# Optimization experiments

Hardware: AMD Instinct MI355X
Metric: run time of the kernel (lower is better)

The kernel has to match this reference:

```python
import jax, jax.numpy as jnp
import numpy as np

N = 50000   # nodes
E = 800000  # edges (avg degree 16)
G = 64      # graphs in batch
H = 4       # attention heads
D = 128     # hidden dim per head (= hidden_dim)
V = 128     # embedding vocab (input_dim)
NEG_SLOPE = 0.2

def setup_inputs() -> dict:
    key = jax.random.key(0)
    ks = jax.random.split(key, 12)
    s = 0.05
    return {
        "feats": jax.random.randint(ks[0], (N,), 0, V),
        "src": jax.random.randint(ks[1], (E,), 0, N),
        "dst": jax.random.randint(ks[2], (E,), 0, N),
        "graph_ids": jnp.sort(jax.random.randint(ks[3], (N,), 0, G)),
        "emb": jax.random.normal(ks[4], (V, D)) * s,
        "W1": jax.random.normal(ks[5], (D, H * D)) * s,
        "b1": jax.random.normal(ks[6], (H * D,)) * s,
        "a1": jax.random.normal(ks[7], (H, D)) * s,
        "W2": jax.random.normal(ks[8], (D, H * D)) * s,
        "b2": jax.random.normal(ks[9], (H * D,)) * s,
        "a2": jax.random.normal(ks[10], (H, D)) * s,
        "Wreg": jax.random.normal(ks[11], (1, D)) * s,
    }

def gatv2_layer(x, W, b, a, src, dst):
    # shared-weight GATv2: h = Wx + b, split into heads -> [N,H,D]
    h = (x @ W + b).reshape(-1, H, D)
    hs = h[src]                      # [E,H,D] source feats per edge
    hd = h[dst]                      # [E,H,D] dest feats per edge
    e = jax.nn.leaky_relu(hs + hd, NEG_SLOPE)
    logits = jnp.einsum('ehd,hd->eh', e, a)          # [E,H]
    # edge softmax over incoming edges of each dst node
    m = jax.ops.segment_max(logits, dst, num_segments=N)
    m = jnp.where(jnp.isfinite(m), m, 0.0)           # empty segments -> 0 (unused)
    ex = jnp.exp(logits - m[dst])
    denom = jax.ops.segment_sum(ex, dst, num_segments=N)
    alpha = ex / denom[dst]                          # [E,H]
    rst = jax.ops.segment_sum(alpha[:, :, None] * hs, dst, num_segments=N)  # [N,H,D]
    return rst.mean(axis=1)          # .mean(dim=1) over heads -> [N,D]

def reference(feats, src, dst, graph_ids, emb, W1, b1, a1, W2, b2, a2, Wreg):
    x = emb[feats]                                   # embedding lookup [N,D]
    x = gatv2_layer(x, W1, b1, a1, src, dst)         # layer 1 (dropout=0)
    x = gatv2_layer(x, W2, b2, a2, src, dst)         # layer 2
    pooled = jax.ops.segment_sum(x, graph_ids, num_segments=G)  # SumPooling [G,D]
    return pooled @ Wreg.T                           # Linear bias=False -> [G,1]
```

## Files before the change

### kernel.cpp

```cpp
#include <hip/hip_runtime.h>
#include <hip/hip_bf16.h>

#define N_NODES 50000
#define N_EDGES 800000
#define G_GRAPHS 64
#define H_HEADS 4
#define D_DIM 128
#define HD 512
#define V_VOCAB 128
#define NEG_SLOPE 0.2f

typedef float f32x2v __attribute__((ext_vector_type(2)));
typedef float f32x4 __attribute__((ext_vector_type(4)));
typedef short s16x8 __attribute__((ext_vector_type(8)));
typedef _Float16 h16x2 __attribute__((ext_vector_type(2)));

static __device__ __forceinline__ float blo(unsigned int u) {
    union { float f; unsigned int i; } x; x.i = u << 16; return x.f;
}
static __device__ __forceinline__ float bhi(unsigned int u) {
    union { float f; unsigned int i; } x; x.i = u & 0xffff0000u; return x.f;
}
static __device__ __forceinline__ unsigned short f2b(float f) {
    union { float f; unsigned int i; } x; x.f = f;
    unsigned int r = x.i + 0x7fffu + ((x.i >> 16) & 1u);
    return (unsigned short)(r >> 16);
}
static __device__ __forceinline__ h16x2 u2h2(unsigned int u) {
    union { unsigned int u; h16x2 h; } c; c.u = u; return c.h;
}
static __device__ __forceinline__ unsigned int h22u(h16x2 h) {
    union { unsigned int u; h16x2 h; } c; c.h = h; return c.u;
}
static __device__ __forceinline__ h16x2 packf2(float lo, float hi) {
    union { __fp16 __attribute__((ext_vector_type(2))) p; h16x2 h; } c;
    c.p = __builtin_amdgcn_cvt_pkrtz(lo, hi);
    return c.h;
}

#if __has_builtin(__builtin_amdgcn_cvt_scalef32_pk_f16_fp8)
static __device__ __forceinline__ void fp8x4_to_h16(unsigned int u, h16x2& h0, h16x2& h1) {
    auto r0 = __builtin_amdgcn_cvt_scalef32_pk_f16_fp8((int)u, 1.0f, false);
    auto r1 = __builtin_amdgcn_cvt_scalef32_pk_f16_fp8((int)u, 1.0f, true);
    union { decltype(r0) p; h16x2 h; } c0, c1;
    c0.p = r0; c1.p = r1;
    h0 = c0.h; h1 = c1.h;
}
#else
static __device__ __forceinline__ void fp8x4_to_h16(unsigned int u, h16x2& h0, h16x2& h1) {
    f32x2v lo = __builtin_amdgcn_cvt_pk_f32_fp8(u, false);
    f32x2v hi = __builtin_amdgcn_cvt_pk_f32_fp8(u, true);
    h0 = packf2(lo.x, lo.y);
    h1 = packf2(hi.x, hi.y);
}
#endif

template<int CTRL>
static __device__ __forceinline__ float dpp_add(float v) {
    union { float f; int i; } a, b;
    a.f = v;
    b.i = __builtin_amdgcn_mov_dpp(a.i, CTRL, 0xF, 0xF, true);
    return v + b.f;
}
static __device__ __forceinline__ float row16_sum(float p) {
    p = dpp_add<0xB1>(p);
    p = dpp_add<0x4E>(p);
    p = dpp_add<0x141>(p);
    p = dpp_add<0x140>(p);
    return p;
}

__global__ void hist_kernel(const int* __restrict__ dst, int* __restrict__ counts,
                            float* __restrict__ pool) {
    if (blockIdx.x == 0 && threadIdx.x < G_GRAPHS) pool[threadIdx.x] = 0.f;
    int i = blockIdx.x * blockDim.x + threadIdx.x;
    if (i < N_EDGES) atomicAdd(&counts[dst[i]], 1);
}

__global__ void __launch_bounds__(256) scan1_kernel(const int* __restrict__ counts,
                                                    int* __restrict__ offsets,
                                                    int* __restrict__ bsum) {
    __shared__ int buf[256];
    int t = threadIdx.x, b = blockIdx.x;
    int i0 = (b * 256 + t) * 4;
    int v[4], c[4], s = 0;
    #pragma unroll
    for (int j = 0; j < 4; j++) {
        int idx = i0 + j;
        v[j] = (idx < N_NODES) ? counts[idx] : 0;
        s += v[j];
        c[j] = s;
    }
    buf[t] = s;
    __syncthreads();
    for (int off = 1; off < 256; off <<= 1) {
        int add = (t >= off) ? buf[t - off] : 0;
        __syncthreads();
        buf[t] += add;
        __syncthreads();
    }
    int ebase = (t > 0) ? buf[t - 1] : 0;
    #pragma unroll
    for (int j = 0; j < 4; j++) {
        int idx = i0 + j;
        if (idx < N_NODES) offsets[idx + 1] = ebase + c[j];
    }
    if (t == 0) bsum[b] = buf[255];
}

__global__ void __launch_bounds__(256) scan23_kernel(const int* __restrict__ counts,
                                                     int* __restrict__ offsets,
                                                     const int* __restrict__ bsum,
                                                     int* __restrict__ cursor) {
    __shared__ int sbase;
    int t = threadIdx.x, b = blockIdx.x;
    if (t < 64) {
        int v = (t < b) ? bsum[t] : 0;
        #pragma unroll
        for (int off = 1; off < 64; off <<= 1) v += __shfl_xor(v, off);
        if (t == 0) sbase = v;
    }
    __syncthreads();
    int base = sbase;
    int i0 = (b * 256 + t) * 4;
    #pragma unroll
    for (int j = 0; j < 4; j++) {
        int idx = i0 + j;
        if (idx < N_NODES) {
            int e = offsets[idx + 1] + base;
            offsets[idx + 1] = e;
            cursor[idx] = e - counts[idx];
        }
    }
    if (b == 0 && t == 0) offsets[0] = 0;
}

__global__ void scatter_kernel(const int* __restrict__ src, const int* __restrict__ dst,
                               int* __restrict__ cursor, int* __restrict__ csr_src) {
    int i = blockIdx.x * blockDim.x + threadIdx.x;
    if (i < N_EDGES) {
        int d = dst[i];
        int pos = atomicAdd(&cursor[d], 1);
        csr_src[pos] = src[i];
    }
}

__global__ void __launch_bounds__(256) prep_kernel(const float* __restrict__ emb,
                                                   const float* __restrict__ W1,
                                                   float* __restrict__ M1,
                                                   const float* __restrict__ W2,
                                                   unsigned short* __restrict__ Wb) {
    int b = blockIdx.x;
    if (b < 256) {
        int idx = b * 256 + threadIdx.x;
        int v = idx >> 9, c = idx & 511;
        float acc = 0.f;
        for (int k = 0; k < 128; k++)
            acc += emb[v * 128 + k] * W1[k * 512 + c];
        M1[idx] = acc;
    } else {
        int idx = (b - 256) * 256 + threadIdx.x;
        int j = idx & 7, c = (idx >> 3) & 511, qq = idx >> 12;
        Wb[idx] = f2b(W2[(qq * 8 + j) * 512 + c]);
    }
}

__global__ void gather_kernel(const int* __restrict__ feats, const float* __restrict__ M1,
                              const float* __restrict__ b1,
                              unsigned int* __restrict__ h) {
    int tid = blockIdx.x * blockDim.x + threadIdx.x;
    int i0 = tid * 8;
    int n = i0 >> 9, c = i0 & 511;
    if (n >= N_NODES) return;
    int f = feats[n];
    const float* mrow = &M1[f * 512 + c];
    float v[8];
    #pragma unroll
    for (int j = 0; j < 8; j++) v[j] = mrow[j] + b1[c + j];
    uint2 o;
    o.x = __builtin_amdgcn_cvt_pk_fp8_f32(v[0], v[1], 0, false);
    o.x = __builtin_amdgcn_cvt_pk_fp8_f32(v[2], v[3], o.x, true);
    o.y = __builtin_amdgcn_cvt_pk_fp8_f32(v[4], v[5], 0, false);
    o.y = __builtin_amdgcn_cvt_pk_fp8_f32(v[6], v[7], o.y, true);
    *reinterpret_cast<uint2*>(&h[i0 >> 2]) = o;
}

template<bool WRITE_DOTS>
__global__ void __launch_bounds__(256) gat_kernel(const unsigned int* __restrict__ h,
                                                  const int* __restrict__ offsets,
                                                  const int* __restrict__ csr_src,
                                                  const float* __restrict__ a,
                                                  const float* __restrict__ wreg,
                                                  unsigned short* __restrict__ x,
                                                  float* __restrict__ dots) {
    int wid = threadIdx.x >> 6;
    int lane = threadIdx.x & 63;
    int n = blockIdx.x * 4 + wid;
    if (n >= N_NODES) return;
    int row_s = offsets[n], row_e = offsets[n + 1];
    int cnt = row_e - row_s;

    h16x2 hd2[4], a06[4], a04[4], acc2[4];
    float pd;
    {
        uint2 hv = *reinterpret_cast<const uint2*>(&h[(size_t)n * 128 + lane * 2]);
        fp8x4_to_h16(hv.x, hd2[0], hd2[1]);
        fp8x4_to_h16(hv.y, hd2[2], hd2[3]);
        float4 av0 = *reinterpret_cast<const float4*>(&a[lane * 8]);
        float4 av1 = *reinterpret_cast<const float4*>(&a[lane * 8 + 4]);
        float aa[8] = {av0.x, av0.y, av0.z, av0.w, av1.x, av1.y, av1.z, av1.w};
        const float L2E = 1.4426950408889634f;
        #pragma unroll
        for (int k = 0; k < 4; k++) {
            a06[k][0] = (_Float16)(aa[2*k]   * (0.6f * L2E));
            a06[k][1] = (_Float16)(aa[2*k+1] * (0.6f * L2E));
            a04[k][0] = (_Float16)(aa[2*k]   * (0.4f * L2E));
            a04[k][1] = (_Float16)(aa[2*k+1] * (0.4f * L2E));
            acc2[k][0] = (_Float16)0.f; acc2[k][1] = (_Float16)0.f;
        }
        float s = 0.f;
        #pragma unroll
        for (int k = 0; k < 4; k++) s = __builtin_amdgcn_fdot2(hd2[k], a06[k], s, false);
        pd = row16_sum(s);
    }

    float den = 0.f;
    uint2 rA = make_uint2(0, 0), rB = make_uint2(0, 0);
    if (cnt > 0) {
        int s = csr_src[row_s];
        rA = *reinterpret_cast<const uint2*>(&h[(size_t)s * 128 + lane * 2]);
    }
    if (cnt > 1) {
        int s = csr_src[row_s + 1];
        rB = *reinterpret_cast<const uint2*>(&h[(size_t)s * 128 + lane * 2]);
    }

    const float C1 = 0.69314718f, C2 = 0.24022651f, C3 = 0.05550411f;

    auto process = [&](uint2 sv) {
        h16x2 hs[4];
        fp8x4_to_h16(sv.x, hs[0], hs[1]);
        fp8x4_to_h16(sv.y, hs[2], hs[3]);
        float p0 = 0.f, p1 = 0.f;
        #pragma unroll
        for (int k = 0; k < 2; k++) {
            h16x2 t2 = hs[k] + hd2[k];
            h16x2 at2 = u2h2(h22u(t2) & 0x7FFF7FFFu);
            p0 = __builtin_amdgcn_fdot2(hs[k], a06[k], p0, false);
            p0 = __builtin_amdgcn_fdot2(at2, a04[k], p0, false);
        }
        #pragma unroll
        for (int k = 2; k < 4; k++) {
            h16x2 t2 = hs[k] + hd2[k];
            h16x2 at2 = u2h2(h22u(t2) & 0x7FFF7FFFu);
            p1 = __builtin_amdgcn_fdot2(hs[k], a06[k], p1, false);
            p1 = __builtin_amdgcn_fdot2(at2, a04[k], p1, false);
        }
        float p = row16_sum(p0 + p1) + pd;
        float w = fmaf(p, fmaf(p, fmaf(p, C3, C2), C1), 1.f);
        den += w;
        h16x2 w2 = packf2(w, w);
        #pragma unroll
        for (int k = 0; k < 4; k++) acc2[k] = w2 * hs[k] + acc2[k];
    };

    for (int i = 0; i < cnt; i += 2) {
        {
            uint2 cur = rA;
            int nx = min(i + 2, cnt - 1);
            int s = csr_src[row_s + nx];
            rA = *reinterpret_cast<const uint2*>(&h[(size_t)s * 128 + lane * 2]);
            process(cur);
        }
        if (i + 1 < cnt) {
            uint2 cur = rB;
            int nx = min(i + 3, cnt - 1);
            int s = csr_src[row_s + nx];
            rB = *reinterpret_cast<const uint2*>(&h[(size_t)s * 128 + lane * 2]);
            process(cur);
        }
    }

    float inv = (den > 0.f) ? 0.25f / den : 0.f;
    float out8[8];
    #pragma unroll
    for (int j = 0; j < 8; j++) {
        float r = (float)acc2[j >> 1][j & 1] * inv;
        r += __shfl_xor(r, 16);
        r += __shfl_xor(r, 32);
        out8[j] = r;
    }
    if constexpr (WRITE_DOTS) {
        int d0 = (lane & 15) * 8;
        float4 wv0 = *reinterpret_cast<const float4*>(&wreg[d0]);
        float4 wv1 = *reinterpret_cast<const float4*>(&wreg[d0 + 4]);
        float pdot = out8[0] * wv0.x + out8[1] * wv0.y + out8[2] * wv0.z + out8[3] * wv0.w
                   + out8[4] * wv1.x + out8[5] * wv1.y + out8[6] * wv1.z + out8[7] * wv1.w;
        pdot = row16_sum(pdot);
        if (lane == 0) dots[n] = pdot;
    } else {
        if (lane < 16) {
            union { unsigned short u[8]; uint4 v; } o;
            #pragma unroll
            for (int j = 0; j < 8; j++) o.u[j] = f2b(out8[j]);
            *reinterpret_cast<uint4*>(&x[(size_t)n * 128 + lane * 8]) = o.v;
        }
    }
}

__global__ void __launch_bounds__(256) gemm_kernel(const unsigned short* __restrict__ x,
                                                   const unsigned short* __restrict__ Wb,
                                                   const float* __restrict__ bias,
                                                   unsigned char* __restrict__ hout) {
    int w = threadIdx.x >> 6, l = threadIdx.x & 63;
    int rb = blockIdx.x * 64 + w * 16;
    int cb = blockIdx.y * 64;
    int lr = l & 15, lq = l >> 4;
    f32x4 acc[4] = {};
    int arow = rb + lr;
    bool rok = arow < N_NODES;
    #pragma unroll
    for (int s = 0; s < 4; s++) {
        s16x8 afr = {};
        if (rok) afr = *reinterpret_cast<const s16x8*>(&x[(size_t)arow * 128 + s * 32 + lq * 8]);
        #pragma unroll
        for (int sub = 0; sub < 4; sub++) {
            s16x8 bfr = *reinterpret_cast<const s16x8*>(
                &Wb[(((size_t)(s * 4 + lq) * 512) + cb + sub * 16 + lr) << 3]);
            acc[sub] = __builtin_amdgcn_mfma_f32_16x16x32_bf16(bfr, afr, acc[sub], 0, 0, 0);
        }
    }
    if (!rok) return;
    #pragma unroll
    for (int sub = 0; sub < 4; sub++) {
        int col0 = cb + sub * 16 + lq * 4;
        float4 bb = *reinterpret_cast<const float4*>(&bias[col0]);
        unsigned int pk = __builtin_amdgcn_cvt_pk_fp8_f32(acc[sub][0] + bb.x,
                                                          acc[sub][1] + bb.y, 0, false);
        pk = __builtin_amdgcn_cvt_pk_fp8_f32(acc[sub][2] + bb.z,
                                             acc[sub][3] + bb.w, pk, true);
        *reinterpret_cast<unsigned int*>(&hout[(size_t)arow * 512 + col0]) = pk;
    }
}

__global__ void __launch_bounds__(256) pool64_kernel(const float* __restrict__ dots,
                                                     const int* __restrict__ gid,
                                                     float* __restrict__ pool) {
    int wave = (blockIdx.x * blockDim.x + threadIdx.x) >> 6;
    int lane = threadIdx.x & 63;
    int n0 = wave * 64;
    if (n0 >= N_NODES) return;
    int n = n0 + lane;
    int nc = min(n, N_NODES - 1);
    int g = gid[nc];
    float v = (n < N_NODES) ? dots[n] : 0.f;
    int g0 = __shfl(g, 0);
    bool uni = __all(g == g0);
    if (uni) {
        v += __shfl_xor(v, 1);
        v += __shfl_xor(v, 2);
        v += __shfl_xor(v, 4);
        v += __shfl_xor(v, 8);
        v += __shfl_xor(v, 16);
        v += __shfl_xor(v, 32);
        if (lane == 0) atomicAdd(&pool[g0], v);
    } else {
        if (n < N_NODES) atomicAdd(&pool[g], v);
    }
}

__global__ void final_kernel(const float* __restrict__ pool, float* __restrict__ out) {
    int t = threadIdx.x;
    if (t < G_GRAPHS) out[t] = pool[t];
}

extern "C" void kernel_launch(void* const* d_in, const int* in_sizes, int n_in,
                              void* d_out, int out_size, void* d_ws, size_t ws_size,
                              hipStream_t stream) {
    const int* feats = (const int*)d_in[0];
    const int* src   = (const int*)d_in[1];
    const int* dst   = (const int*)d_in[2];
    const int* gids  = (const int*)d_in[3];
    const float* emb  = (const float*)d_in[4];
    const float* W1   = (const float*)d_in[5];
    const float* b1   = (const float*)d_in[6];
    const float* a1   = (const float*)d_in[7];
    const float* W2   = (const float*)d_in[8];
    const float* b2   = (const float*)d_in[9];
    const float* a2   = (const float*)d_in[10];
    const float* wreg = (const float*)d_in[11];
    float* out = (float*)d_out;

    char* ws = (char*)d_ws;
    size_t off = 0;
    auto alloc = [&](size_t bytes) -> void* {
        void* p = ws + off;
        off = (off + bytes + 255) & ~(size_t)255;
        return p;
    };
    int*   counts  = (int*)alloc((size_t)N_NODES * 4);
    int*   offsets = (int*)alloc((size_t)(N_NODES + 1) * 4);
    int*   cursor  = (int*)alloc((size_t)N_NODES * 4);
    int*   csr_src = (int*)alloc((size_t)N_EDGES * 4);
    int*   bsum    = (int*)alloc(64 * 4);
    float* M1      = (float*)alloc((size_t)V_VOCAB * HD * 4);
    unsigned int*   h  = (unsigned int*)alloc((size_t)N_NODES * HD);
    unsigned short* x  = (unsigned short*)alloc((size_t)N_NODES * D_DIM * 2);
    unsigned short* Wb = (unsigned short*)alloc((size_t)D_DIM * HD * 2);
    float* dots    = (float*)alloc((size_t)N_NODES * 4);
    float* pool    = (float*)alloc((size_t)G_GRAPHS * 4);

    hipMemsetAsync(counts, 0, (size_t)N_NODES * 4, stream);

    hist_kernel<<<(N_EDGES + 255) / 256, 256, 0, stream>>>(dst, counts, pool);
    scan1_kernel<<<64, 256, 0, stream>>>(counts, offsets, bsum);
    scan23_kernel<<<64, 256, 0, stream>>>(counts, offsets, bsum, cursor);
    scatter_kernel<<<(N_EDGES + 255) / 256, 256, 0, stream>>>(src, dst, cursor, csr_src);

    prep_kernel<<<512, 256, 0, stream>>>(emb, W1, M1, W2, Wb);
    gather_kernel<<<(N_NODES * HD / 8) / 256, 256, 0, stream>>>(feats, M1, b1, h);

    gat_kernel<false><<<(N_NODES + 3) / 4, 256, 0, stream>>>(h, offsets, csr_src, a1,
                                                             wreg, x, dots);
    gemm_kernel<<<dim3((N_NODES + 63) / 64, 8), 256, 0, stream>>>(x, Wb, b2, (unsigned char*)h);
    gat_kernel<true><<<(N_NODES + 3) / 4, 256, 0, stream>>>(h, offsets, csr_src, a2,
                                                            wreg, x, dots);

    pool64_kernel<<<(N_NODES / 64 + 4) / 4, 256, 0, stream>>>(dots, gids, pool);
    final_kernel<<<1, 64, 0, stream>>>(pool, out);
}
```

Before: 362.9 us.

## Fold memset into prep kernel, fuse final copy into pool, scalarize GAT indices

Replaces the hipMemsetAsync of counts with extra blocks in prep_kernel, which is moved ahead of the histogram. It removes final_kernel by having the last block of pool64_kernel (found with an atomic done counter) write the output. In gat_kernel the node index, row offsets and neighbor indices become wave-uniform through readfirstlane, and 32-bit address math replaces size_t. Together these cut launch count and per-edge vector address work, at the cost of an atomic counter plus threadfence in the pooling kernel.

```diff
diff --git a/kernel.cpp b/kernel.cpp
--- a/kernel.cpp
+++ b/kernel.cpp
@@ -15,12 +15,6 @@
 typedef short s16x8 __attribute__((ext_vector_type(8)));
 typedef _Float16 h16x2 __attribute__((ext_vector_type(2)));
 
-static __device__ __forceinline__ float blo(unsigned int u) {
-    union { float f; unsigned int i; } x; x.i = u << 16; return x.f;
-}
-static __device__ __forceinline__ float bhi(unsigned int u) {
-    union { float f; unsigned int i; } x; x.i = u & 0xffff0000u; return x.f;
-}
 static __device__ __forceinline__ unsigned short f2b(float f) {
     union { float f; unsigned int i; } x; x.f = f;
     unsigned int r = x.i + 0x7fffu + ((x.i >> 16) & 1u);
@@ -145,23 +139,32 @@
     }
 }
 
+#define PREP_M1_BLOCKS   256
+#define PREP_WSZ_BLOCKS  256
+#define PREP_CNT_BLOCKS  196
 __global__ void __launch_bounds__(256) prep_kernel(const float* __restrict__ emb,
                                                    const float* __restrict__ W1,
                                                    float* __restrict__ M1,
                                                    const float* __restrict__ W2,
-                                                   unsigned short* __restrict__ Wb) {
+                                                   unsigned short* __restrict__ Wb,
+                                                   int* __restrict__ counts,
+                                                   int* __restrict__ done) {
     int b = blockIdx.x;
-    if (b < 256) {
+    if (b < PREP_M1_BLOCKS) {
         int idx = b * 256 + threadIdx.x;
         int v = idx >> 9, c = idx & 511;
         float acc = 0.f;
         for (int k = 0; k < 128; k++)
             acc += emb[v * 128 + k] * W1[k * 512 + c];
         M1[idx] = acc;
-    } else {
-        int idx = (b - 256) * 256 + threadIdx.x;
+    } else if (b < PREP_M1_BLOCKS + PREP_WSZ_BLOCKS) {
+        int idx = (b - PREP_M1_BLOCKS) * 256 + threadIdx.x;
         int j = idx & 7, c = (idx >> 3) & 511, qq = idx >> 12;
         Wb[idx] = f2b(W2[(qq * 8 + j) * 512 + c]);
+    } else {
+        int idx = (b - PREP_M1_BLOCKS - PREP_WSZ_BLOCKS) * 256 + threadIdx.x;
+        if (idx < N_NODES) counts[idx] = 0;
+        if (idx == 0) *done = 0;
     }
 }
 
@@ -197,13 +200,16 @@
     int lane = threadIdx.x & 63;
     int n = blockIdx.x * 4 + wid;
     if (n >= N_NODES) return;
-    int row_s = offsets[n], row_e = offsets[n + 1];
+    n = __builtin_amdgcn_readfirstlane(n);
+    int row_s = __builtin_amdgcn_readfirstlane(offsets[n]);
+    int row_e = __builtin_amdgcn_readfirstlane(offsets[n + 1]);
     int cnt = row_e - row_s;
+    int voff = lane * 2;
 
     h16x2 hd2[4], a06[4], a04[4], acc2[4];
     float pd;
     {
-        uint2 hv = *reinterpret_cast<const uint2*>(&h[(size_t)n * 128 + lane * 2]);
+        uint2 hv = *reinterpret_cast<const uint2*>(&h[(unsigned)n * 128u + voff]);
         fp8x4_to_h16(hv.x, hd2[0], hd2[1]);
         fp8x4_to_h16(hv.y, hd2[2], hd2[3]);
         float4 av0 = *reinterpret_cast<const float4*>(&a[lane * 8]);
@@ -224,16 +230,15 @@
         pd = row16_sum(s);
     }
 
+    auto ld = [&](int ii) {
+        int s = __builtin_amdgcn_readfirstlane(csr_src[row_s + ii]);
+        return *reinterpret_cast<const uint2*>(&h[(unsigned)s * 128u + voff]);
+    };
+
     float den = 0.f;
     uint2 rA = make_uint2(0, 0), rB = make_uint2(0, 0);
-    if (cnt > 0) {
-        int s = csr_src[row_s];
-        rA = *reinterpret_cast<const uint2*>(&h[(size_t)s * 128 + lane * 2]);
-    }
-    if (cnt > 1) {
-        int s = csr_src[row_s + 1];
-        rB = *reinterpret_cast<const uint2*>(&h[(size_t)s * 128 + lane * 2]);
-    }
+    if (cnt > 0) rA = ld(0);
+    if (cnt > 1) rB = ld(1);
 
     const float C1 = 0.69314718f, C2 = 0.24022651f, C3 = 0.05550411f;
 
@@ -267,16 +272,12 @@
     for (int i = 0; i < cnt; i += 2) {
         {
             uint2 cur = rA;
-            int nx = min(i + 2, cnt - 1);
-            int s = csr_src[row_s + nx];
-            rA = *reinterpret_cast<const uint2*>(&h[(size_t)s * 128 + lane * 2]);
+            rA = ld(min(i + 2, cnt - 1));
             process(cur);
         }
         if (i + 1 < cnt) {
             uint2 cur = rB;
-            int nx = min(i + 3, cnt - 1);
-            int s = csr_src[row_s + nx];
-            rB = *reinterpret_cast<const uint2*>(&h[(size_t)s * 128 + lane * 2]);
+            rB = ld(min(i + 3, cnt - 1));
             process(cur);
         }
     }
@@ -303,7 +304,7 @@
             union { unsigned short u[8]; uint4 v; } o;
             #pragma unroll
             for (int j = 0; j < 8; j++) o.u[j] = f2b(out8[j]);
-            *reinterpret_cast<uint4*>(&x[(size_t)n * 128 + lane * 8]) = o.v;
+            *reinterpret_cast<uint4*>(&x[(unsigned)n * 128u + lane * 8]) = o.v;
         }
     }
 }
@@ -345,33 +346,40 @@
 
 __global__ void __launch_bounds__(256) pool64_kernel(const float* __restrict__ dots,
                                                      const int* __restrict__ gid,
-                                                     float* __restrict__ pool) {
+                                                     float* __restrict__ pool,
+                                                     int* __restrict__ done,
+                                                     float* __restrict__ out) {
     int wave = (blockIdx.x * blockDim.x + threadIdx.x) >> 6;
     int lane = threadIdx.x & 63;
     int n0 = wave * 64;
-    if (n0 >= N_NODES) return;
-    int n = n0 + lane;
-    int nc = min(n, N_NODES - 1);
-    int g = gid[nc];
-    float v = (n < N_NODES) ? dots[n] : 0.f;
-    int g0 = __shfl(g, 0);
-    bool uni = __all(g == g0);
-    if (uni) {
-        v += __shfl_xor(v, 1);
-        v += __shfl_xor(v, 2);
-        v += __shfl_xor(v, 4);
-        v += __shfl_xor(v, 8);
-        v += __shfl_xor(v, 16);
-        v += __shfl_xor(v, 32);
-        if (lane == 0) atomicAdd(&pool[g0], v);
-    } else {
-        if (n < N_NODES) atomicAdd(&pool[g], v);
-    }
-}
-
-__global__ void final_kernel(const float* __restrict__ pool, float* __restrict__ out) {
-    int t = threadIdx.x;
-    if (t < G_GRAPHS) out[t] = pool[t];
+    if (n0 < N_NODES) {
+        int n = n0 + lane;
+        int nc = min(n, N_NODES - 1);
+        int g = gid[nc];
+        float v = (n < N_NODES) ? dots[n] : 0.f;
+        int g0 = __shfl(g, 0);
+        bool uni = __all(g == g0);
+        if (uni) {
+            v += __shfl_xor(v, 1);
+            v += __shfl_xor(v, 2);
+            v += __shfl_xor(v, 4);
+            v += __shfl_xor(v, 8);
+            v += __shfl_xor(v, 16);
+            v += __shfl_xor(v, 32);
+            if (lane == 0) atomicAdd(&pool[g0], v);
+        } else {
+            if (n < N_NODES) atomicAdd(&pool[g], v);
+        }
+    }
+    __threadfence();
+    __syncthreads();
+    __shared__ int amlast;
+    if (threadIdx.x == 0)
+        amlast = (atomicAdd(done, 1) == (int)gridDim.x - 1) ? 1 : 0;
+    __syncthreads();
+    if (amlast && threadIdx.x < G_GRAPHS) {
+        out[threadIdx.x] = atomicAdd(&pool[threadIdx.x], 0.f);
+    }
 }
 
 extern "C" void kernel_launch(void* const* d_in, const int* in_sizes, int n_in,
@@ -403,6 +411,7 @@
     int*   cursor  = (int*)alloc((size_t)N_NODES * 4);
     int*   csr_src = (int*)alloc((size_t)N_EDGES * 4);
     int*   bsum    = (int*)alloc(64 * 4);
+    int*   done    = (int*)alloc(4);
     float* M1      = (float*)alloc((size_t)V_VOCAB * HD * 4);
     unsigned int*   h  = (unsigned int*)alloc((size_t)N_NODES * HD);
     unsigned short* x  = (unsigned short*)alloc((size_t)N_NODES * D_DIM * 2);
@@ -410,14 +419,13 @@
     float* dots    = (float*)alloc((size_t)N_NODES * 4);
     float* pool    = (float*)alloc((size_t)G_GRAPHS * 4);
 
-    hipMemsetAsync(counts, 0, (size_t)N_NODES * 4, stream);
-
+    prep_kernel<<<PREP_M1_BLOCKS + PREP_WSZ_BLOCKS + PREP_CNT_BLOCKS, 256, 0, stream>>>(
+        emb, W1, M1, W2, Wb, counts, done);
     hist_kernel<<<(N_EDGES + 255) / 256, 256, 0, stream>>>(dst, counts, pool);
     scan1_kernel<<<64, 256, 0, stream>>>(counts, offsets, bsum);
     scan23_kernel<<<64, 256, 0, stream>>>(counts, offsets, bsum, cursor);
     scatter_kernel<<<(N_EDGES + 255) / 256, 256, 0, stream>>>(src, dst, cursor, csr_src);
 
-    prep_kernel<<<512, 256, 0, stream>>>(emb, W1, M1, W2, Wb);
     gather_kernel<<<(N_NODES * HD / 8) / 256, 256, 0, stream>>>(feats, M1, b1, h);
 
     gat_kernel<false><<<(N_NODES + 3) / 4, 256, 0, stream>>>(h, offsets, csr_src, a1,
@@ -426,6 +434,5 @@
     gat_kernel<true><<<(N_NODES + 3) / 4, 256, 0, stream>>>(h, offsets, csr_src, a2,
                                                             wreg, x, dots);
 
-    pool64_kernel<<<(N_NODES / 64 + 4) / 4, 256, 0, stream>>>(dots, gids, pool);
-    final_kernel<<<1, 64, 0, stream>>>(pool, out);
-}
+    pool64_kernel<<<(N_NODES / 64 + 4) / 4, 256, 0, stream>>>(dots, gids, pool, done, out);
+}
```

Measured after the change: 335.2 us. -7.6%, faster.
